# Optimization experiments

Hardware: AMD Instinct MI355X
Metric: run time of the kernel (lower is better)

## Reference

```python
import jax, jax.numpy as jnp
import numpy as np

B, C, H_IMG, W_IMG = 16, 384, 56, 56
NUM_HEADS = 6
HEAD_DIM = C // NUM_HEADS
BN_EPS = 1e-5


def _bn(x, gamma, beta, mean, var):
    # x: [b, ch, n] or [b, ch, h, w]; per-channel affine normalization (eval-mode BatchNorm)
    shape = (1, -1) + (1,) * (x.ndim - 2)
    scale = (gamma / jnp.sqrt(var + BN_EPS)).reshape(shape)
    shift = (beta - mean * gamma / jnp.sqrt(var + BN_EPS)).reshape(shape)
    return x * scale + shift


def setup_inputs() -> dict:
    key = jax.random.key(0)
    ks = jax.random.split(key, 12)
    c2 = 2 * C
    return {
        "x": jax.random.normal(ks[0], (B, C, H_IMG, W_IMG), jnp.float32),
        "qk_w": jax.random.normal(ks[1], (c2, C // 2), jnp.float32) * 0.05,
        "qk_gamma": jax.random.uniform(ks[2], (c2,), jnp.float32, 0.5, 1.5),
        "qk_beta": jax.random.normal(ks[3], (c2,), jnp.float32) * 0.1,
        "qk_mean": jax.random.normal(ks[4], (c2,), jnp.float32) * 0.1,
        "qk_var": jax.random.uniform(ks[5], (c2,), jnp.float32, 0.5, 1.5),
        "pe_w": jax.random.normal(ks[6], (C, 1, 3, 3), jnp.float32) * 0.1,
        "pe_gamma": jax.random.uniform(ks[7], (C,), jnp.float32, 0.5, 1.5),
        "pe_beta": jax.random.normal(ks[8], (C,), jnp.float32) * 0.1,
        "pe_mean": jax.random.normal(ks[9], (C,), jnp.float32) * 0.1,
        "pe_var": jax.random.uniform(ks[10], (C,), jnp.float32, 0.5, 1.5),
    }


def reference(x, qk_w, qk_gamma, qk_beta, qk_mean, qk_var,
              pe_w, pe_gamma, pe_beta, pe_mean, pe_var):
    b, c, h, w = x.shape
    n = h * w
    s = n ** (-0.5)
    nh, hd = NUM_HEADS, HEAD_DIM

    # grouped (groups=2) 1x1 conv: out channels [0:c] from input [0:c/2], [c:2c] from [c/2:c]
    xg = x.reshape(b, 2, c // 2, n)                       # [b, 2, c/2, n]
    wg = qk_w.reshape(2, c, c // 2)                       # [group, out_per_group, in_per_group]
    qk = jnp.einsum('bgin,goi->bgon', xg, wg).reshape(b, 2 * c, n)
    qk = _bn(qk, qk_gamma, qk_beta, qk_mean, qk_var)
    qk = jax.nn.elu(qk) + 1.0

    qk = qk.reshape(b, 2, nh, hd, n)
    q, k = qk[:, 0], qk[:, 1]                             # [b, H, d, n]
    v = x.reshape(b, nh, hd, n)                           # [b, H, d, n]

    # kv = (k*s) @ (v^T * s): [b, H, d, d]
    kv = jnp.einsum('bhdn,bhen->bhde', k * s, v * s)
    # numerator: q^T @ kv -> [b, H, n, d]
    num = jnp.einsum('bhdn,bhde->bhne', q, kv)
    # denominator: q^T @ mean_n(k) -> [b, H, n]
    den = jnp.einsum('bhdn,bhd->bhn', q, k.mean(axis=-1)) + 1e-6
    attn = (num / den[..., None]).transpose(0, 1, 3, 2).reshape(b, c, h, w)

    # depthwise 3x3 conv positional encoding on v (= x) + BN
    pe = jax.lax.conv_general_dilated(
        x, pe_w, window_strides=(1, 1), padding=((1, 1), (1, 1)),
        feature_group_count=c, dimension_numbers=('NCHW', 'OIHW', 'NCHW'))
    pe = _bn(pe, pe_gamma, pe_beta, pe_mean, pe_var)

    return attn + pe
```

## Files before the change

### kernel.cpp

```cpp
#include <hip/hip_runtime.h>
#include <math.h>

#define N_SP 3136
#define BN_EPS 1e-5f

typedef __attribute__((ext_vector_type(8))) short short8;
typedef __attribute__((ext_vector_type(4))) float f32x4;

#define K_SZ    (16*384*N_SP)
#define QF_OFF  (K_SZ)
#define QF_FSZ  (16*6*49*8192/2)
#define KVP_OFF (QF_OFF + QF_FSZ)
#define KVP_SZ  (16*6*7*64*80)
#define KVT_OFF (KVP_OFF + KVP_SZ)
#define KVT_FSZ (2*96*80*64/2)
#define WH_OFF  (KVT_OFF + KVT_FSZ)
#define WSPLIT_N (2*384*192)

#define FSWZ(n) ((((n) >> 1) ^ ((n) >> 2)) & 7)

__device__ __forceinline__ void bsplit(float f, ushort& h, ushort& l) {
    uint u = __float_as_uint(f);
    uint hr = (u + 0x7FFFu + ((u >> 16) & 1u)) >> 16;
    h = (ushort)hr;
    float fh = __uint_as_float(hr << 16);
    float fl = f - fh;
    uint v = __float_as_uint(fl);
    l = (ushort)((v + 0x7FFFu + ((v >> 16) & 1u)) >> 16);
}

__global__ __launch_bounds__(256) void p0_wsplit(
    const float* __restrict__ qk_w, ushort* __restrict__ wh, ushort* __restrict__ wl)
{
    int idx = blockIdx.x * 256 + threadIdx.x;
    if (idx >= WSPLIT_N) return;
    ushort h, l;
    bsplit(qk_w[idx], h, l);
    wh[idx] = h;
    wl[idx] = l;
}

__global__ __launch_bounds__(256) void k0_pe(
    const float* __restrict__ x, const float* __restrict__ pw,
    const float* __restrict__ pgamma, const float* __restrict__ pbeta,
    const float* __restrict__ pmean, const float* __restrict__ pvar,
    float* __restrict__ out)
{
    const int bc = blockIdx.x;
    const int cc = bc % 384;
    const float* xp = x + (size_t)bc * N_SP;
    float* op = out + (size_t)bc * N_SP;
    float w9[9];
    #pragma unroll
    for (int q = 0; q < 9; ++q) w9[q] = pw[cc * 9 + q];
    float sc = pgamma[cc] / sqrtf(pvar[cc] + BN_EPS);
    float sh = pbeta[cc] - pmean[cc] * sc;

    for (int s = threadIdx.x; s < 392; s += 256) {
        int y = s / 7, xs = (s % 7) * 8;
        float row[3][10];
        #pragma unroll
        for (int dy = 0; dy < 3; ++dy) {
            int yy = y + dy - 1;
            bool yok = (yy >= 0) && (yy < 56);
            if (yok) {
                const float* xr = xp + yy * 56;
                float4 a = *(const float4*)&xr[xs];
                float4 bq = *(const float4*)&xr[xs + 4];
                row[dy][1] = a.x;  row[dy][2] = a.y;  row[dy][3] = a.z;  row[dy][4] = a.w;
                row[dy][5] = bq.x; row[dy][6] = bq.y; row[dy][7] = bq.z; row[dy][8] = bq.w;
                row[dy][0] = (xs > 0)  ? xr[xs - 1] : 0.f;
                row[dy][9] = (xs < 48) ? xr[xs + 8] : 0.f;
            } else {
                #pragma unroll
                for (int i = 0; i < 10; ++i) row[dy][i] = 0.f;
            }
        }
        float ov[8];
        #pragma unroll
        for (int p = 0; p < 8; ++p) {
            float conv = 0.f;
            #pragma unroll
            for (int dy = 0; dy < 3; ++dy)
                #pragma unroll
                for (int dx = 0; dx < 3; ++dx)
                    conv += w9[dy * 3 + dx] * row[dy][p + dx];
            ov[p] = conv * sc + sh;
        }
        float* po = op + y * 56 + xs;
        *(float4*)po = make_float4(ov[0], ov[1], ov[2], ov[3]);
        *(float4*)(po + 4) = make_float4(ov[4], ov[5], ov[6], ov[7]);
    }
}

__global__ __launch_bounds__(256) void k1_qk_mfma(
    const float* __restrict__ x, const ushort* __restrict__ wh, const ushort* __restrict__ wl,
    const float* __restrict__ gamma, const float* __restrict__ beta,
    const float* __restrict__ mean, const float* __restrict__ var,
    uint* __restrict__ kq, ushort* __restrict__ qf)
{
    __shared__ __align__(16) ushort Ah[8192];
    __shared__ __align__(16) ushort Al[8192];
    __shared__ __align__(16) ushort Bh[4096];
    __shared__ __align__(16) ushort Bl[4096];

    const int bx = blockIdx.x;
    const int by = blockIdx.y;
    const int bz = blockIdx.z;
    const int b = bz >> 1, gg = bz & 1;
    const int t = threadIdx.x;
    const int lane = t & 63, wv = t >> 6;
    const int wr = wv >> 1, wc = wv & 1;
    const int lg = lane >> 4, l15 = lane & 15;

    f32x4 acc[4][2];
    #pragma unroll
    for (int m = 0; m < 4; ++m)
        #pragma unroll
        for (int nf = 0; nf < 2; ++nf)
            acc[m][nf] = (f32x4){0.f, 0.f, 0.f, 0.f};

    const float* xg = x + (size_t)(b * 384 + gg * 192) * N_SP + bx * 64;
    const ushort* whg = wh + (gg * 384 + by * 128) * 192;
    const ushort* wlg = wl + (gg * 384 + by * 128) * 192;

    for (int kt = 0; kt < 3; ++kt) {
        #pragma unroll
        for (int li = 0; li < 4; ++li) {
            int c = li * 256 + t;
            int row = c >> 3, kb = c & 7;
            int goff = row * 192 + kt * 64 + kb * 8;
            float4 vh = *(const float4*)(whg + goff);
            float4 vl = *(const float4*)(wlg + goff);
            int ch = (row * 8 + (kb ^ (row & 7))) * 8;
            *(float4*)&Ah[ch] = vh;
            *(float4*)&Al[ch] = vl;
        }
        #pragma unroll
        for (int li = 0; li < 2; ++li) {
            int idx = li * 256 + t;
            int kp = idx >> 4;
            int nq = idx & 15;
            int k0 = kp * 2;
            const float* px = xg + (size_t)(kt * 64 + k0) * N_SP + nq * 4;
            float4 v0 = *(const float4*)px;
            float4 v1 = *(const float4*)(px + N_SP);
            ushort h0[4], l0[4], h1[4], l1[4];
            float a0[4] = {v0.x, v0.y, v0.z, v0.w};
            float a1[4] = {v1.x, v1.y, v1.z, v1.w};
            #pragma unroll
            for (int i = 0; i < 4; ++i) { bsplit(a0[i], h0[i], l0[i]); bsplit(a1[i], h1[i], l1[i]); }
            int kb = k0 >> 3, ks = (k0 & 6) >> 1;
            #pragma unroll
            for (int i = 0; i < 4; ++i) {
                int n = nq * 4 + i;
                int chunk = n * 8 + (kb ^ FSWZ(n));
                ((uint*)Bh)[chunk * 4 + ks] = (uint)h0[i] | ((uint)h1[i] << 16);
                ((uint*)Bl)[chunk * 4 + ks] = (uint)l0[i] | ((uint)l1[i] << 16);
            }
        }
        __syncthreads();
        #pragma unroll
        for (int s = 0; s < 2; ++s) {
            short8 ah[4], al[4], bh[2], bl[2];
            int kb = s * 4 + lg;
            #pragma unroll
            for (int m = 0; m < 4; ++m) {
                int row = wr * 64 + m * 16 + l15;
                int ch = (row * 8 + (kb ^ (row & 7))) * 8;
                ah[m] = *(const short8*)&Ah[ch];
                al[m] = *(const short8*)&Al[ch];
            }
            #pragma unroll
            for (int nf = 0; nf < 2; ++nf) {
                int n = wc * 32 + nf * 16 + l15;
                int ch = (n * 8 + (kb ^ FSWZ(n))) * 8;
                bh[nf] = *(const short8*)&Bh[ch];
                bl[nf] = *(const short8*)&Bl[ch];
            }
            #pragma unroll
            for (int m = 0; m < 4; ++m)
                #pragma unroll
                for (int nf = 0; nf < 2; ++nf) {
                    acc[m][nf] = __builtin_amdgcn_mfma_f32_16x16x32_bf16(ah[m], bh[nf], acc[m][nf], 0, 0, 0);
                    acc[m][nf] = __builtin_amdgcn_mfma_f32_16x16x32_bf16(ah[m], bl[nf], acc[m][nf], 0, 0, 0);
                    acc[m][nf] = __builtin_amdgcn_mfma_f32_16x16x32_bf16(al[m], bh[nf], acc[m][nf], 0, 0, 0);
                }
        }
        __syncthreads();
    }

    float* scs = (float*)Bh;
    float* shs = scs + 128;
    if (t < 128) {
        int ch = gg * 384 + by * 128 + t;
        float sc = gamma[ch] / sqrtf(var[ch] + BN_EPS);
        scs[t] = sc;
        shs[t] = beta[ch] - mean[ch] * sc;
    }
    __syncthreads();

    if (gg == 0) {
        const int head = by * 2 + wr;
        ushort* qbase = qf + ((size_t)(b * 6 + head) * 49 + bx) * 8192;
        #pragma unroll
        for (int m = 0; m < 4; ++m) {
            #pragma unroll
            for (int nf = 0; nf < 2; ++nf) {
                ushort hh[4], ll[4];
                #pragma unroll
                for (int r = 0; r < 4; ++r) {
                    int orow = wr * 64 + m * 16 + lg * 4 + r;
                    float v = acc[m][nf][r] * scs[orow] + shs[orow];
                    v = v > 0.f ? v + 1.f : __expf(v);
                    bsplit(v, hh[r], ll[r]);
                }
                int hc = m * 4 + lg;
                int n = wc * 32 + nf * 16 + l15;
                uint2 uh, ul;
                uh.x = (uint)hh[0] | ((uint)hh[1] << 16);
                uh.y = (uint)hh[2] | ((uint)hh[3] << 16);
                ul.x = (uint)ll[0] | ((uint)ll[1] << 16);
                ul.y = (uint)ll[2] | ((uint)ll[3] << 16);
                *(uint2*)(qbase + (size_t)hc * 256 + n * 4) = uh;
                *(uint2*)(qbase + (size_t)(16 + hc) * 256 + n * 4) = ul;
            }
        }
    } else {
        size_t obase = ((size_t)b * 384 + by * 128) * N_SP + bx * 64 + wc * 32;
        #pragma unroll
        for (int m = 0; m < 4; ++m)
            #pragma unroll
            for (int nf = 0; nf < 2; ++nf) {
                #pragma unroll
                for (int r = 0; r < 4; ++r) {
                    int orow = wr * 64 + m * 16 + lg * 4 + r;
                    float v = acc[m][nf][r] * scs[orow] + shs[orow];
                    v = v > 0.f ? v + 1.f : __expf(v);
                    ushort hh, ll;
                    bsplit(v, hh, ll);
                    kq[obase + (size_t)orow * N_SP + nf * 16 + l15] = (uint)hh | ((uint)ll << 16);
                }
            }
    }
}

__global__ __launch_bounds__(256) void k2_kv_mfma(
    const float* __restrict__ x, const uint* __restrict__ kq,
    float* __restrict__ kv_part)
{
    __shared__ __align__(16) ushort Kh[4096], Kl[4096];
    __shared__ __align__(16) ushort Vh[5120], Vl[5120];

    const int chunk = blockIdx.x;
    const int h = blockIdx.y, b = blockIdx.z;
    const int t = threadIdx.x;
    const int lane = t & 63, wv = t >> 6;
    const int lg = lane >> 4, l15 = lane & 15;

    const uint* kp  = kq + (size_t)(b*384 + h*64) * N_SP;
    const float* vp = x  + (size_t)(b*384 + h*64) * N_SP;

    #pragma unroll
    for (int li = 0; li < 4; ++li) {
        int idx = li * 256 + t;
        int row = 64 + (idx >> 6), col = idx & 63;
        int off = (row * 8 + ((col >> 3) ^ (row & 7))) * 8 + (col & 7);
        Vh[off] = (row == 64) ? (ushort)0x3F80 : (ushort)0;
        Vl[off] = 0;
    }

    f32x4 acc[5];
    #pragma unroll
    for (int nf = 0; nf < 5; ++nf) acc[nf] = (f32x4){0.f, 0.f, 0.f, 0.f};

    for (int sub = 0; sub < 7; ++sub) {
        int n0 = chunk * 448 + sub * 64;
        #pragma unroll
        for (int li = 0; li < 4; ++li) {
            int idx = li * 256 + t;
            int row = idx >> 4, sc = idx & 15;
            int off = (row * 8 + ((sc >> 1) ^ (row & 7))) * 8 + (sc & 1) * 4;
            uint4 kf = *(const uint4*)&kp[(size_t)row * N_SP + n0 + sc * 4];
            ((uint*)&Kh[off])[0] = (kf.x & 0xFFFFu) | (kf.y << 16);
            ((uint*)&Kh[off])[1] = (kf.z & 0xFFFFu) | (kf.w << 16);
            ((uint*)&Kl[off])[0] = (kf.x >> 16) | (kf.y & 0xFFFF0000u);
            ((uint*)&Kl[off])[1] = (kf.z >> 16) | (kf.w & 0xFFFF0000u);
            float4 vf = *(const float4*)&vp[(size_t)row * N_SP + n0 + sc * 4];
            ushort h0,h1,h2,h3,l0,l1,l2,l3;
            bsplit(vf.x,h0,l0); bsplit(vf.y,h1,l1); bsplit(vf.z,h2,l2); bsplit(vf.w,h3,l3);
            ((uint*)&Vh[off])[0] = (uint)h0 | ((uint)h1 << 16);
            ((uint*)&Vh[off])[1] = (uint)h2 | ((uint)h3 << 16);
            ((uint*)&Vl[off])[0] = (uint)l0 | ((uint)l1 << 16);
            ((uint*)&Vl[off])[1] = (uint)l2 | ((uint)l3 << 16);
        }
        __syncthreads();
        #pragma unroll
        for (int s = 0; s < 2; ++s) {
            int arow = wv * 16 + l15;
            int akb = (s * 4 + lg) ^ (arow & 7);
            short8 ah = *(const short8*)&Kh[(arow * 8 + akb) * 8];
            short8 al = *(const short8*)&Kl[(arow * 8 + akb) * 8];
            #pragma unroll
            for (int nf = 0; nf < 5; ++nf) {
                int brow = nf * 16 + l15;
                int bkb = (s * 4 + lg) ^ (brow & 7);
                short8 bh = *(const short8*)&Vh[(brow * 8 + bkb) * 8];
                short8 bl = *(const short8*)&Vl[(brow * 8 + bkb) * 8];
                acc[nf] = __builtin_amdgcn_mfma_f32_16x16x32_bf16(ah, bh, acc[nf], 0, 0, 0);
                acc[nf] = __builtin_amdgcn_mfma_f32_16x16x32_bf16(ah, bl, acc[nf], 0, 0, 0);
                acc[nf] = __builtin_amdgcn_mfma_f32_16x16x32_bf16(al, bh, acc[nf], 0, 0, 0);
            }
        }
        __syncthreads();
    }

    size_t base = (size_t)((b*6 + h)*7 + chunk) * 64 * 80;
    #pragma unroll
    for (int nf = 0; nf < 5; ++nf)
        #pragma unroll
        for (int r = 0; r < 4; ++r) {
            int d = wv * 16 + lg * 4 + r;
            kv_part[base + (size_t)d * 80 + nf * 16 + l15] = acc[nf][r];
        }
}

__global__ __launch_bounds__(256) void k2b_reduce(
    const float* __restrict__ kv_part,
    ushort* __restrict__ kvt_h, ushort* __restrict__ kvt_l)
{
    const int bh = blockIdx.x;
    const int t = threadIdx.x;
    const float inv_n = 1.0f / (float)N_SP;
    const float* base = kv_part + (size_t)bh * 7 * 5120;
    ushort* oh = kvt_h + (size_t)bh * 5120;
    ushort* ol = kvt_l + (size_t)bh * 5120;
    float s[20];
    #pragma unroll
    for (int j = 0; j < 20; ++j) s[j] = 0.f;
    for (int c = 0; c < 7; ++c) {
        #pragma unroll
        for (int j = 0; j < 20; ++j) s[j] += base[c * 5120 + j * 256 + t];
    }
    #pragma unroll
    for (int j = 0; j < 20; ++j) {
        int i = j * 256 + t;
        int d = i / 80, e = i % 80;
        ushort h, l;
        bsplit(s[j] * inv_n, h, l);
        oh[e * 64 + d] = h;
        ol[e * 64 + d] = l;
    }
}

__device__ __forceinline__ void load_qfrag(const ushort* qtile, int wv, int lg, int l15,
                                           short8* qh, short8* ql)
{
    #pragma unroll
    for (int s = 0; s < 2; ++s) {
        int hc = (s * 4 + lg) * 2;
        const ushort* ph = qtile + hc * 256 + (wv * 16 + l15) * 4;
        uint2 a0 = *(const uint2*)ph;
        uint2 a1 = *(const uint2*)(ph + 256);
        uint* bh = (uint*)&qh[s];
        bh[0] = a0.x; bh[1] = a0.y; bh[2] = a1.x; bh[3] = a1.y;
        const ushort* pl = ph + 16 * 256;
        uint2 c0 = *(const uint2*)pl;
        uint2 c1 = *(const uint2*)(pl + 256);
        uint* bl = (uint*)&ql[s];
        bl[0] = c0.x; bl[1] = c0.y; bl[2] = c1.x; bl[3] = c1.y;
    }
}

#define ATT_STRIDE 68
__global__ __launch_bounds__(256) void k3a_attn(
    const ushort* __restrict__ qf,
    const ushort* __restrict__ kvt_h, const ushort* __restrict__ kvt_l,
    float* __restrict__ out)
{
    __shared__ __align__(16) float SBF[ATT_STRIDE * 64 + 64];

    const int bx = blockIdx.x;
    const int h = blockIdx.y, b = blockIdx.z;
    const int t = threadIdx.x;
    const int lane = t & 63, wv = t >> 6;
    const int lg = lane >> 4, l15 = lane & 15;
    const int n0 = bx * 64;

    const ushort* qtile = qf + ((size_t)(b * 6 + h) * 49 + bx) * 8192;
    short8 bqh[2], bql[2];
    load_qfrag(qtile, wv, lg, l15, bqh, bql);

    const ushort* ahb = kvt_h + (size_t)(b * 6 + h) * 5120;
    const ushort* alb = kvt_l + (size_t)(b * 6 + h) * 5120;
    f32x4 acc[5];
    #pragma unroll
    for (int m = 0; m < 5; ++m) acc[m] = (f32x4){0.f, 0.f, 0.f, 0.f};
    #pragma unroll
    for (int s = 0; s < 2; ++s) {
        #pragma unroll
        for (int m = 0; m < 5; ++m) {
            int off = (m * 16 + l15) * 64 + (s * 4 + lg) * 8;
            short8 ah = *(const short8*)&ahb[off];
            short8 al = *(const short8*)&alb[off];
            acc[m] = __builtin_amdgcn_mfma_f32_16x16x32_bf16(ah, bqh[s], acc[m], 0, 0, 0);
            acc[m] = __builtin_amdgcn_mfma_f32_16x16x32_bf16(ah, bql[s], acc[m], 0, 0, 0);
            acc[m] = __builtin_amdgcn_mfma_f32_16x16x32_bf16(al, bqh[s], acc[m], 0, 0, 0);
        }
    }

    {
        int ncol = wv * 16 + l15;
        #pragma unroll
        for (int m = 0; m < 4; ++m)
            #pragma unroll
            for (int r = 0; r < 4; ++r)
                SBF[(m * 16 + lg * 4 + r) * ATT_STRIDE + ncol] = acc[m][r];
        if (lg == 0)
            SBF[ATT_STRIDE * 64 + ncol] = acc[4][0];
    }
    __syncthreads();

    const int tx = t & 15, ty = t >> 4;
    const int p0 = n0 + tx * 4;
    float den[4];
    #pragma unroll
    for (int p = 0; p < 4; ++p) den[p] = SBF[ATT_STRIDE * 64 + tx * 4 + p] + 1e-6f;
    #pragma unroll
    for (int j = 0; j < 4; ++j) {
        int cc = ty * 4 + j;
        int c = h * 64 + cc;
        float* po = &out[((size_t)b * 384 + c) * N_SP + p0];
        float4 pe = *(const float4*)po;
        const float* pep = (const float*)&pe;
        float4 r;
        float* pr = (float*)&r;
        #pragma unroll
        for (int p = 0; p < 4; ++p)
            pr[p] = SBF[cc * ATT_STRIDE + tx * 4 + p] / den[p] + pep[p];
        *(float4*)po = r;
    }
}

extern "C" void kernel_launch(void* const* d_in, const int* in_sizes, int n_in,
                              void* d_out, int out_size, void* d_ws, size_t ws_size,
                              hipStream_t stream)
{
    const float* x        = (const float*)d_in[0];
    const float* qk_w     = (const float*)d_in[1];
    const float* qk_gamma = (const float*)d_in[2];
    const float* qk_beta  = (const float*)d_in[3];
    const float* qk_mean  = (const float*)d_in[4];
    const float* qk_var   = (const float*)d_in[5];
    const float* pe_w     = (const float*)d_in[6];
    const float* pe_gamma = (const float*)d_in[7];
    const float* pe_beta  = (const float*)d_in[8];
    const float* pe_mean  = (const float*)d_in[9];
    const float* pe_var   = (const float*)d_in[10];
    float* out = (float*)d_out;

    float* ws      = (float*)d_ws;
    uint* kq       = (uint*)ws;
    ushort* qf     = (ushort*)(ws + QF_OFF);
    float* kv_part = ws + KVP_OFF;
    ushort* kvt_h  = (ushort*)(ws + KVT_OFF);
    ushort* kvt_l  = kvt_h + 96 * 5120;
    ushort* whp    = (ushort*)(ws + WH_OFF);
    ushort* wlp    = whp + WSPLIT_N;

    hipLaunchKernelGGL(p0_wsplit, dim3((WSPLIT_N + 255)/256), dim3(256), 0, stream,
                       qk_w, whp, wlp);
    hipLaunchKernelGGL(k0_pe, dim3(6144), dim3(256), 0, stream,
                       x, pe_w, pe_gamma, pe_beta, pe_mean, pe_var, out);
    dim3 g1(49, 3, 32);
    hipLaunchKernelGGL(k1_qk_mfma, g1, dim3(256), 0, stream,
                       x, whp, wlp, qk_gamma, qk_beta, qk_mean, qk_var, kq, qf);
    dim3 g2(7, 6, 16);
    hipLaunchKernelGGL(k2_kv_mfma, g2, dim3(256), 0, stream, x, kq, kv_part);
    hipLaunchKernelGGL(k2b_reduce, dim3(96), dim3(256), 0, stream,
                       kv_part, kvt_h, kvt_l);
    dim3 g3(49, 6, 16);
    hipLaunchKernelGGL(k3a_attn, g3, dim3(256), 0, stream,
                       qf, kvt_h, kvt_l, out);
}
```

Baseline: 242.8 us.

## Compute all 384 qk output channels per block, staging the full x tile once

The QK projection kernel now has each block compute all 384 output channels of a group for a 64-column spatial tile, instead of 128 channels over three K iterations. The full 192-deep x tile is converted once into LDS with a new swizzle. Weight fragments are read straight from global memory (L2-cached) rather than staged through LDS. This removes the threefold re-reading and re-splitting of x across the channel-block grid dimension and drops the intermediate barriers. In exchange each wave holds 96 accumulator registers (6x4 fragments), which lowers occupancy, the grid shrinks to 1568 blocks, and uncoalesced global weight loads may add latency.

After: 263.4 us. +8.5%, slower.

```diff
diff --git a/kernel.cpp b/kernel.cpp
--- a/kernel.cpp
+++ b/kernel.cpp
@@ -17,7 +17,7 @@
 #define WH_OFF  (KVT_OFF + KVT_FSZ)
 #define WSPLIT_N (2*384*192)
 
-#define FSWZ(n) ((((n) >> 1) ^ ((n) >> 2)) & 7)
+#define FSWZ2(n) (((n) ^ ((n) >> 3)) & 7)
 
 __device__ __forceinline__ void bsplit(float f, ushort& h, ushort& l) {
     uint u = __float_as_uint(f);
@@ -99,124 +99,102 @@
     const float* __restrict__ mean, const float* __restrict__ var,
     uint* __restrict__ kq, ushort* __restrict__ qf)
 {
-    __shared__ __align__(16) ushort Ah[8192];
-    __shared__ __align__(16) ushort Al[8192];
-    __shared__ __align__(16) ushort Bh[4096];
-    __shared__ __align__(16) ushort Bl[4096];
+    __shared__ __align__(16) ushort Bh[12288];
+    __shared__ __align__(16) ushort Bl[12288];
+    __shared__ float scs[384], shs[384];
 
     const int bx = blockIdx.x;
-    const int by = blockIdx.y;
-    const int bz = blockIdx.z;
+    const int bz = blockIdx.y;
     const int b = bz >> 1, gg = bz & 1;
     const int t = threadIdx.x;
     const int lane = t & 63, wv = t >> 6;
-    const int wr = wv >> 1, wc = wv & 1;
     const int lg = lane >> 4, l15 = lane & 15;
 
-    f32x4 acc[4][2];
-    #pragma unroll
-    for (int m = 0; m < 4; ++m)
-        #pragma unroll
-        for (int nf = 0; nf < 2; ++nf)
-            acc[m][nf] = (f32x4){0.f, 0.f, 0.f, 0.f};
-
     const float* xg = x + (size_t)(b * 384 + gg * 192) * N_SP + bx * 64;
-    const ushort* whg = wh + (gg * 384 + by * 128) * 192;
-    const ushort* wlg = wl + (gg * 384 + by * 128) * 192;
-
-    for (int kt = 0; kt < 3; ++kt) {
-        #pragma unroll
-        for (int li = 0; li < 4; ++li) {
-            int c = li * 256 + t;
-            int row = c >> 3, kb = c & 7;
-            int goff = row * 192 + kt * 64 + kb * 8;
-            float4 vh = *(const float4*)(whg + goff);
-            float4 vl = *(const float4*)(wlg + goff);
-            int ch = (row * 8 + (kb ^ (row & 7))) * 8;
-            *(float4*)&Ah[ch] = vh;
-            *(float4*)&Al[ch] = vl;
-        }
-        #pragma unroll
-        for (int li = 0; li < 2; ++li) {
-            int idx = li * 256 + t;
-            int kp = idx >> 4;
-            int nq = idx & 15;
-            int k0 = kp * 2;
-            const float* px = xg + (size_t)(kt * 64 + k0) * N_SP + nq * 4;
-            float4 v0 = *(const float4*)px;
-            float4 v1 = *(const float4*)(px + N_SP);
-            ushort h0[4], l0[4], h1[4], l1[4];
-            float a0[4] = {v0.x, v0.y, v0.z, v0.w};
-            float a1[4] = {v1.x, v1.y, v1.z, v1.w};
-            #pragma unroll
-            for (int i = 0; i < 4; ++i) { bsplit(a0[i], h0[i], l0[i]); bsplit(a1[i], h1[i], l1[i]); }
-            int kb = k0 >> 3, ks = (k0 & 6) >> 1;
-            #pragma unroll
-            for (int i = 0; i < 4; ++i) {
-                int n = nq * 4 + i;
-                int chunk = n * 8 + (kb ^ FSWZ(n));
-                ((uint*)Bh)[chunk * 4 + ks] = (uint)h0[i] | ((uint)h1[i] << 16);
-                ((uint*)Bl)[chunk * 4 + ks] = (uint)l0[i] | ((uint)l1[i] << 16);
+    const ushort* whg = wh + gg * 384 * 192;
+    const ushort* wlg = wl + gg * 384 * 192;
+
+    #pragma unroll
+    for (int li = 0; li < 6; ++li) {
+        int idx = li * 256 + t;
+        int kp = idx >> 4;
+        int nq = idx & 15;
+        int k0 = kp * 2;
+        const float* px = xg + (size_t)k0 * N_SP + nq * 4;
+        float4 v0 = *(const float4*)px;
+        float4 v1 = *(const float4*)(px + N_SP);
+        ushort h0[4], l0[4], h1[4], l1[4];
+        float a0[4] = {v0.x, v0.y, v0.z, v0.w};
+        float a1[4] = {v1.x, v1.y, v1.z, v1.w};
+        #pragma unroll
+        for (int i = 0; i < 4; ++i) { bsplit(a0[i], h0[i], l0[i]); bsplit(a1[i], h1[i], l1[i]); }
+        int kb = k0 >> 3, ks = kp & 3;
+        #pragma unroll
+        for (int i = 0; i < 4; ++i) {
+            int n = nq * 4 + i;
+            int chunk = n * 24 + (kb ^ FSWZ2(n));
+            ((uint*)Bh)[chunk * 4 + ks] = (uint)h0[i] | ((uint)h1[i] << 16);
+            ((uint*)Bl)[chunk * 4 + ks] = (uint)l0[i] | ((uint)l1[i] << 16);
+        }
+    }
+    for (int i = t; i < 384; i += 256) {
+        int ch = gg * 384 + i;
+        float sc = gamma[ch] / sqrtf(var[ch] + BN_EPS);
+        scs[i] = sc;
+        shs[i] = beta[ch] - mean[ch] * sc;
+    }
+    __syncthreads();
+
+    f32x4 acc[6][4];
+    #pragma unroll
+    for (int mf = 0; mf < 6; ++mf)
+        #pragma unroll
+        for (int nf = 0; nf < 4; ++nf)
+            acc[mf][nf] = (f32x4){0.f, 0.f, 0.f, 0.f};
+
+    for (int s = 0; s < 6; ++s) {
+        int kb = s * 4 + lg;
+        short8 bh[4], bl[4];
+        #pragma unroll
+        for (int nf = 0; nf < 4; ++nf) {
+            int n = nf * 16 + l15;
+            int chunk = n * 24 + (kb ^ FSWZ2(n));
+            bh[nf] = *(const short8*)&Bh[chunk * 8];
+            bl[nf] = *(const short8*)&Bl[chunk * 8];
+        }
+        #pragma unroll
+        for (int mf = 0; mf < 6; ++mf) {
+            int row = wv * 96 + mf * 16 + l15;
+            int goff = row * 192 + kb * 8;
+            short8 ah = *(const short8*)&whg[goff];
+            short8 al = *(const short8*)&wlg[goff];
+            #pragma unroll
+            for (int nf = 0; nf < 4; ++nf) {
+                acc[mf][nf] = __builtin_amdgcn_mfma_f32_16x16x32_bf16(ah, bh[nf], acc[mf][nf], 0, 0, 0);
+                acc[mf][nf] = __builtin_amdgcn_mfma_f32_16x16x32_bf16(ah, bl[nf], acc[mf][nf], 0, 0, 0);
+                acc[mf][nf] = __builtin_amdgcn_mfma_f32_16x16x32_bf16(al, bh[nf], acc[mf][nf], 0, 0, 0);
             }
         }
-        __syncthreads();
-        #pragma unroll
-        for (int s = 0; s < 2; ++s) {
-            short8 ah[4], al[4], bh[2], bl[2];
-            int kb = s * 4 + lg;
-            #pragma unroll
-            for (int m = 0; m < 4; ++m) {
-                int row = wr * 64 + m * 16 + l15;
-                int ch = (row * 8 + (kb ^ (row & 7))) * 8;
-                ah[m] = *(const short8*)&Ah[ch];
-                al[m] = *(const short8*)&Al[ch];
-            }
-            #pragma unroll
-            for (int nf = 0; nf < 2; ++nf) {
-                int n = wc * 32 + nf * 16 + l15;
-                int ch = (n * 8 + (kb ^ FSWZ(n))) * 8;
-                bh[nf] = *(const short8*)&Bh[ch];
-                bl[nf] = *(const short8*)&Bl[ch];
-            }
-            #pragma unroll
-            for (int m = 0; m < 4; ++m)
-                #pragma unroll
-                for (int nf = 0; nf < 2; ++nf) {
-                    acc[m][nf] = __builtin_amdgcn_mfma_f32_16x16x32_bf16(ah[m], bh[nf], acc[m][nf], 0, 0, 0);
-                    acc[m][nf] = __builtin_amdgcn_mfma_f32_16x16x32_bf16(ah[m], bl[nf], acc[m][nf], 0, 0, 0);
-                    acc[m][nf] = __builtin_amdgcn_mfma_f32_16x16x32_bf16(al[m], bh[nf], acc[m][nf], 0, 0, 0);
-                }
-        }
-        __syncthreads();
-    }
-
-    float* scs = (float*)Bh;
-    float* shs = scs + 128;
-    if (t < 128) {
-        int ch = gg * 384 + by * 128 + t;
-        float sc = gamma[ch] / sqrtf(var[ch] + BN_EPS);
-        scs[t] = sc;
-        shs[t] = beta[ch] - mean[ch] * sc;
-    }
-    __syncthreads();
+    }
 
     if (gg == 0) {
-        const int head = by * 2 + wr;
-        ushort* qbase = qf + ((size_t)(b * 6 + head) * 49 + bx) * 8192;
-        #pragma unroll
-        for (int m = 0; m < 4; ++m) {
-            #pragma unroll
-            for (int nf = 0; nf < 2; ++nf) {
+        #pragma unroll
+        for (int mf = 0; mf < 6; ++mf) {
+            int rbase = wv * 96 + mf * 16 + lg * 4;
+            int head = rbase >> 6;
+            int hc = (rbase & 63) >> 2;
+            ushort* qbase = qf + ((size_t)(b * 6 + head) * 49 + bx) * 8192;
+            #pragma unroll
+            for (int nf = 0; nf < 4; ++nf) {
                 ushort hh[4], ll[4];
                 #pragma unroll
                 for (int r = 0; r < 4; ++r) {
-                    int orow = wr * 64 + m * 16 + lg * 4 + r;
-                    float v = acc[m][nf][r] * scs[orow] + shs[orow];
+                    int orow = rbase + r;
+                    float v = acc[mf][nf][r] * scs[orow] + shs[orow];
                     v = v > 0.f ? v + 1.f : __expf(v);
                     bsplit(v, hh[r], ll[r]);
                 }
-                int hc = m * 4 + lg;
-                int n = wc * 32 + nf * 16 + l15;
+                int n = nf * 16 + l15;
                 uint2 uh, ul;
                 uh.x = (uint)hh[0] | ((uint)hh[1] << 16);
                 uh.y = (uint)hh[2] | ((uint)hh[3] << 16);
@@ -227,15 +205,15 @@
             }
         }
     } else {
-        size_t obase = ((size_t)b * 384 + by * 128) * N_SP + bx * 64 + wc * 32;
-        #pragma unroll
-        for (int m = 0; m < 4; ++m)
-            #pragma unroll
-            for (int nf = 0; nf < 2; ++nf) {
+        size_t obase = (size_t)b * 384 * N_SP + bx * 64;
+        #pragma unroll
+        for (int mf = 0; mf < 6; ++mf)
+            #pragma unroll
+            for (int nf = 0; nf < 4; ++nf) {
                 #pragma unroll
                 for (int r = 0; r < 4; ++r) {
-                    int orow = wr * 64 + m * 16 + lg * 4 + r;
-                    float v = acc[m][nf][r] * scs[orow] + shs[orow];
+                    int orow = wv * 96 + mf * 16 + lg * 4 + r;
+                    float v = acc[mf][nf][r] * scs[orow] + shs[orow];
                     v = v > 0.f ? v + 1.f : __expf(v);
                     ushort hh, ll;
                     bsplit(v, hh, ll);
@@ -472,7 +450,7 @@
                        qk_w, whp, wlp);
     hipLaunchKernelGGL(k0_pe, dim3(6144), dim3(256), 0, stream,
                        x, pe_w, pe_gamma, pe_beta, pe_mean, pe_var, out);
-    dim3 g1(49, 3, 32);
+    dim3 g1(49, 32);
     hipLaunchKernelGGL(k1_qk_mfma, g1, dim3(256), 0, stream,
                        x, whp, wlp, qk_gamma, qk_beta, qk_mean, qk_var, kq, qf);
     dim3 g2(7, 6, 16);
```
